# Kernel tuning notes

Hardware: AMD Instinct MI355X
Metric: run time of the kernel (lower is better)

Reference implementation:

```python
import jax, jax.numpy as jnp
import numpy as np

EMB_DIM = 1024
NUM_HEADS = 16
HEAD_DIM = EMB_DIM // NUM_HEADS
B, S = 2, 2048


def setup_inputs() -> dict:
    key = jax.random.key(0)
    k1, k2, k3, k4, k5, k6 = jax.random.split(key, 6)
    query = jax.random.normal(k1, (B, S, EMB_DIM), dtype=jnp.float32)
    key_t = jax.random.normal(k2, (B, S, EMB_DIM), dtype=jnp.float32)
    # causal mask: True above the diagonal = masked
    attention_mask = jnp.triu(jnp.ones((S, S), dtype=bool), k=1)
    scale = 1.0 / np.sqrt(EMB_DIM)
    Wq = jax.random.normal(k3, (EMB_DIM, EMB_DIM), dtype=jnp.float32) * scale
    Wk = jax.random.normal(k4, (EMB_DIM, EMB_DIM), dtype=jnp.float32) * scale
    Wv = jax.random.normal(k5, (EMB_DIM, EMB_DIM), dtype=jnp.float32) * scale
    Wo = jax.random.normal(k6, (EMB_DIM, EMB_DIM), dtype=jnp.float32) * scale
    return {"query": query, "key": key_t, "attention_mask": attention_mask,
            "Wq": Wq, "Wk": Wk, "Wv": Wv, "Wo": Wo}


def _split_heads(x):
    b, s, d = x.shape
    return x.reshape(b, s, NUM_HEADS, HEAD_DIM).transpose(0, 2, 1, 3)  # [B,H,S,hd]


def reference(query, key, attention_mask, Wq, Wk, Wv, Wo):
    # self-attention (encoder_decoder_attention=False): k,v come from query; `key` unused
    q = _split_heads(query @ Wq.T)
    k = _split_heads(query @ Wk.T)
    v = _split_heads(query @ Wv.T)
    scores = jnp.einsum('bhqd,bhkd->bhqk', q, k) / np.sqrt(HEAD_DIM)
    # causal=True: mask broadcast as [1,1,S,S]
    scores = jnp.where(attention_mask[None, None, :, :], -jnp.inf, scores)
    attn_weights = jax.nn.softmax(scores, axis=-1)  # [B,H,S,S]
    # dropout p=0.0 -> identity
    attn_out = jnp.einsum('bhqk,bhkd->bhqd', attn_weights, v)
    attn_out = attn_out.transpose(0, 2, 1, 3).reshape(query.shape[0], query.shape[1], EMB_DIM)
    attn_out = attn_out @ Wo.T
    return attn_out, attn_weights
```

## Files before the change

kernel.cpp:

```cpp
#include <hip/hip_runtime.h>
#include <stdint.h>

typedef __attribute__((ext_vector_type(8))) short bf16x8;
typedef __attribute__((ext_vector_type(4))) float f32x4;

#define MFMA16(a, b, c) __builtin_amdgcn_mfma_f32_16x16x32_bf16((a), (b), (c), 0, 0, 0)

static constexpr int NH = 16, HD = 64, SEQ = 2048, EMB = 1024;
static constexpr size_t O0 = (size_t)2 * SEQ * EMB;

__device__ __forceinline__ ushort f2bf(float f) {
  union { float f; uint32_t u; } v; v.f = f;
  uint32_t u = v.u;
  u = (u + 0x7fffu + ((u >> 16) & 1u)) >> 16;
  return (ushort)u;
}
__device__ __forceinline__ float bf2f(ushort h) {
  union { uint32_t u; float f; } v; v.u = ((uint32_t)h) << 16; return v.f;
}

__global__ void detect_kernel(const ushort* __restrict__ X, int* flag) {
  __shared__ int cnt;
  if (threadIdx.x == 0) cnt = 0;
  __syncthreads();
  int ok = 0;
  for (int i = 0; i < 16; ++i) {
    ushort w = X[threadIdx.x * 16 + i];
    int e = (w >> 7) & 0xFF;
    ok += (w == 0 || (e >= 100 && e <= 140)) ? 1 : 0;
  }
  atomicAdd(&cnt, ok);
  __syncthreads();
  if (threadIdx.x == 0) *flag = (cnt >= 3700) ? 0 : 1;
}

__global__ __launch_bounds__(256) void convert5(const void* __restrict__ x,
                                                const void* __restrict__ wq,
                                                const void* __restrict__ wk,
                                                const void* __restrict__ wv,
                                                const void* __restrict__ wo,
                                                ushort* __restrict__ Xb,
                                                ushort* __restrict__ Wb,
                                                const int* __restrict__ flagp) {
  const bool in32 = (*flagp) != 0;
  const size_t M = (size_t)1 << 20;
  const size_t gid = ((size_t)blockIdx.x * 256 + threadIdx.x) * 16;
  const void* src; ushort* dst; size_t off;
  if (gid < 4 * M)      { src = x;  off = gid;         dst = Xb + gid; }
  else if (gid < 5 * M) { src = wq; off = gid - 4 * M; dst = Wb + (gid - 4 * M); }
  else if (gid < 6 * M) { src = wk; off = gid - 5 * M; dst = Wb + (gid - 4 * M); }
  else if (gid < 7 * M) { src = wv; off = gid - 6 * M; dst = Wb + (gid - 4 * M); }
  else                  { src = wo; off = gid - 7 * M; dst = Wb + (gid - 4 * M); }
  if (in32) {
    const float4* p = reinterpret_cast<const float4*>((const float*)src + off);
    union { ushort h[16]; uint4 v[2]; } u;
#pragma unroll
    for (int j = 0; j < 4; ++j) {
      float4 fq = p[j];
      u.h[j * 4 + 0] = f2bf(fq.x); u.h[j * 4 + 1] = f2bf(fq.y);
      u.h[j * 4 + 2] = f2bf(fq.z); u.h[j * 4 + 3] = f2bf(fq.w);
    }
    *reinterpret_cast<uint4*>(dst)     = u.v[0];
    *reinterpret_cast<uint4*>(dst + 8) = u.v[1];
  } else {
    const uint4* p = reinterpret_cast<const uint4*>((const ushort*)src + off);
    *reinterpret_cast<uint4*>(dst)     = p[0];
    *reinterpret_cast<uint4*>(dst + 8) = p[1];
  }
}

__global__ __launch_bounds__(256, 3) void proj_qkv(const ushort* __restrict__ X,
                                                   const ushort* __restrict__ Wq,
                                                   const ushort* __restrict__ Wk,
                                                   const ushort* __restrict__ Wv,
                                                   ushort* __restrict__ Qws,
                                                   ushort* __restrict__ Kws,
                                                   ushort* __restrict__ Vtws) {
  __shared__ ushort As[128 * 72];
  __shared__ ushort Bs[128 * 72];
  const int t = threadIdx.x;
  const int wave = t >> 6, lane = t & 63, quad = lane >> 4, lr = lane & 15;
  const int wm = wave >> 1, wn = wave & 1;
  const int mBase = blockIdx.y * 128;
  const int nGlob = blockIdx.x * 128;
  const int which = nGlob >> 10;
  const int nBase = nGlob & 1023;
  const ushort* W = (which == 0) ? Wq : (which == 1) ? Wk : Wv;
  ushort* outp = (which == 0) ? Qws : (which == 1) ? Kws : Vtws;

  f32x4 acc[4][4];
  const f32x4 z4 = {0.f, 0.f, 0.f, 0.f};
#pragma unroll
  for (int mi = 0; mi < 4; ++mi)
#pragma unroll
    for (int ni = 0; ni < 4; ++ni) acc[mi][ni] = z4;

  for (int kb = 0; kb < 16; ++kb) {
    __syncthreads();
#pragma unroll
    for (int i = 0; i < 4; ++i) {
      int id = t + i * 256, r = id >> 3, c = id & 7;
      *reinterpret_cast<uint4*>(&As[r * 72 + c * 8]) =
          *reinterpret_cast<const uint4*>(X + (size_t)(mBase + r) * 1024 + kb * 64 + c * 8);
      *reinterpret_cast<uint4*>(&Bs[r * 72 + c * 8]) =
          *reinterpret_cast<const uint4*>(W + (size_t)(nBase + r) * 1024 + kb * 64 + c * 8);
    }
    __syncthreads();
#pragma unroll
    for (int ks = 0; ks < 2; ++ks) {
      bf16x8 af[4], bfr[4];
#pragma unroll
      for (int mi = 0; mi < 4; ++mi)
        af[mi] = *reinterpret_cast<const bf16x8*>(
            &As[(wm * 64 + mi * 16 + lr) * 72 + ks * 32 + quad * 8]);
#pragma unroll
      for (int ni = 0; ni < 4; ++ni)
        bfr[ni] = *reinterpret_cast<const bf16x8*>(
            &Bs[(wn * 64 + ni * 16 + lr) * 72 + ks * 32 + quad * 8]);
#pragma unroll
      for (int mi = 0; mi < 4; ++mi)
#pragma unroll
        for (int ni = 0; ni < 4; ++ni)
          acc[mi][ni] = MFMA16(af[mi], bfr[ni], acc[mi][ni]);
    }
  }

#pragma unroll
  for (int mi = 0; mi < 4; ++mi)
#pragma unroll
    for (int ni = 0; ni < 4; ++ni)
#pragma unroll
      for (int reg = 0; reg < 4; ++reg) {
        int m = mBase + wm * 64 + mi * 16 + quad * 4 + reg;
        int n = nBase + wn * 64 + ni * 16 + lr;
        int b = m >> 11, s = m & 2047, h = n >> 6, d = n & 63;
        size_t idx = (which == 2)
            ? ((size_t)(b * NH + h) * HD + d) * SEQ + s
            : ((size_t)(b * NH + h) * SEQ + s) * HD + d;
        outp[idx] = f2bf(acc[mi][ni][reg]);
      }
}

__global__ __launch_bounds__(256, 4) void proj_out(const ushort* __restrict__ A,
                                                   const ushort* __restrict__ W,
                                                   void* __restrict__ outp,
                                                   const int* __restrict__ flagp) {
  __shared__ ushort As[64 * 72];
  __shared__ ushort Bs[128 * 72];
  const bool f32io = (*flagp) != 0;
  const int t = threadIdx.x;
  const int wave = t >> 6, lane = t & 63, quad = lane >> 4, lr = lane & 15;
  const int wm = wave >> 1, wn = wave & 1;
  const int mBase = blockIdx.y * 64, nBase = blockIdx.x * 128;

  f32x4 acc[2][4];
  const f32x4 z4 = {0.f, 0.f, 0.f, 0.f};
#pragma unroll
  for (int mi = 0; mi < 2; ++mi)
#pragma unroll
    for (int ni = 0; ni < 4; ++ni) acc[mi][ni] = z4;

  for (int kb = 0; kb < 16; ++kb) {
    __syncthreads();
#pragma unroll
    for (int i = 0; i < 2; ++i) {
      int id = t + i * 256, r = id >> 3, c = id & 7;
      *reinterpret_cast<uint4*>(&As[r * 72 + c * 8]) =
          *reinterpret_cast<const uint4*>(A + (size_t)(mBase + r) * 1024 + kb * 64 + c * 8);
    }
#pragma unroll
    for (int i = 0; i < 4; ++i) {
      int id = t + i * 256, r = id >> 3, c = id & 7;
      *reinterpret_cast<uint4*>(&Bs[r * 72 + c * 8]) =
          *reinterpret_cast<const uint4*>(W + (size_t)(nBase + r) * 1024 + kb * 64 + c * 8);
    }
    __syncthreads();
#pragma unroll
    for (int ks = 0; ks < 2; ++ks) {
      bf16x8 af[2], bfr[4];
#pragma unroll
      for (int mi = 0; mi < 2; ++mi)
        af[mi] = *reinterpret_cast<const bf16x8*>(
            &As[(wm * 32 + mi * 16 + lr) * 72 + ks * 32 + quad * 8]);
#pragma unroll
      for (int ni = 0; ni < 4; ++ni)
        bfr[ni] = *reinterpret_cast<const bf16x8*>(
            &Bs[(wn * 64 + ni * 16 + lr) * 72 + ks * 32 + quad * 8]);
#pragma unroll
      for (int mi = 0; mi < 2; ++mi)
#pragma unroll
        for (int ni = 0; ni < 4; ++ni)
          acc[mi][ni] = MFMA16(af[mi], bfr[ni], acc[mi][ni]);
    }
  }

#pragma unroll
  for (int mi = 0; mi < 2; ++mi)
#pragma unroll
    for (int ni = 0; ni < 4; ++ni)
#pragma unroll
      for (int reg = 0; reg < 4; ++reg) {
        int m = mBase + wm * 32 + mi * 16 + quad * 4 + reg;
        int n = nBase + wn * 64 + ni * 16 + lr;
        size_t idx = (size_t)m * EMB + n;
        if (f32io) ((float*)outp)[idx] = acc[mi][ni][reg];
        else       ((ushort*)outp)[idx] = f2bf(acc[mi][ni][reg]);
      }
}

__global__ __launch_bounds__(256, 4) void attn_kernel(const ushort* __restrict__ Q,
                                                      const ushort* __restrict__ K,
                                                      const ushort* __restrict__ Vt,
                                                      void* __restrict__ dout,
                                                      ushort* __restrict__ Oout,
                                                      const int* __restrict__ flagp) {
  __shared__ ushort KVs[128 * 72];
  __shared__ ushort Ps[64 * 136];

  const int f = *flagp;
  const int t = threadIdx.x;
  const int wave = t >> 6, lane = t & 63, quad = lane >> 4, lr = lane & 15;
  const int bh = blockIdx.x, b = bh >> 4, h = bh & 15;
  const int sel = blockIdx.y, g = sel >> 3, r8 = sel & 7;
  const int qt = g * 8 + ((g & 1) ? r8 : 7 - r8);
  const int qBase = qt * 64;
  const int lastkt = qBase >> 7;

  const ushort* Qp = Q + (size_t)bh * SEQ * HD;
  const ushort* Kp = K + (size_t)bh * SEQ * HD;
  const ushort* Vp = Vt + (size_t)bh * HD * SEQ;
  ushort* P16 = (ushort*)dout + O0 + (size_t)bh * SEQ * SEQ;
  float*  P32 = (float*)dout + O0 + (size_t)bh * SEQ * SEQ;

#pragma unroll
  for (int i = 0; i < 2; ++i) {
    int id = t + i * 256, r = id >> 3, c = id & 7;
    *reinterpret_cast<uint4*>(&Ps[r * 72 + c * 8]) =
        *reinterpret_cast<const uint4*>(Qp + (size_t)(qBase + r) * HD + c * 8);
  }
  __syncthreads();
  bf16x8 qa[2];
#pragma unroll
  for (int ks = 0; ks < 2; ++ks)
    qa[ks] = *reinterpret_cast<const bf16x8*>(
        &Ps[(wave * 16 + lr) * 72 + ks * 32 + quad * 8]);

  if (f) {
    const float4 zf = make_float4(0.f, 0.f, 0.f, 0.f);
    for (int zt = lastkt + 1; zt < 16; ++zt)
#pragma unroll
      for (int i = 0; i < 8; ++i) {
        int id = t + i * 256, r = id >> 5, c = id & 31;
        *reinterpret_cast<float4*>(P32 + (size_t)(qBase + r) * SEQ + zt * 128 + c * 4) = zf;
      }
  } else {
    const uint4 zz = make_uint4(0, 0, 0, 0);
    for (int zt = lastkt + 1; zt < 16; ++zt)
#pragma unroll
      for (int i = 0; i < 4; ++i) {
        int id = t + i * 256, r = id >> 4, c = id & 15;
        *reinterpret_cast<uint4*>(P16 + (size_t)(qBase + r) * SEQ + zt * 128 + c * 8) = zz;
      }
  }

  float m_i[4], l_i[4], rl[4];
#pragma unroll
  for (int reg = 0; reg < 4; ++reg) { m_i[reg] = -1e9f; l_i[reg] = 0.f; }
  f32x4 oacc[4];
  const f32x4 z4 = {0.f, 0.f, 0.f, 0.f};
#pragma unroll
  for (int ni = 0; ni < 4; ++ni) oacc[ni] = z4;

  for (int pass = 0; pass < 2; ++pass) {
    if (pass == 1) {
#pragma unroll
      for (int reg = 0; reg < 4; ++reg) rl[reg] = 1.f / l_i[reg];
    }
    for (int kt = 0; kt <= lastkt; ++kt) {
      __syncthreads();
#pragma unroll
      for (int i = 0; i < 4; ++i) {
        int id = t + i * 256, r = id >> 3, c = id & 7;
        *reinterpret_cast<uint4*>(&KVs[r * 72 + c * 8]) =
            *reinterpret_cast<const uint4*>(Kp + (size_t)(kt * 128 + r) * HD + c * 8);
      }
      __syncthreads();

      f32x4 s[8];
#pragma unroll
      for (int ni = 0; ni < 8; ++ni) s[ni] = z4;
#pragma unroll
      for (int ni = 0; ni < 8; ++ni) {
        bf16x8 kb0 = *reinterpret_cast<const bf16x8*>(&KVs[(ni * 16 + lr) * 72 + quad * 8]);
        bf16x8 kb1 = *reinterpret_cast<const bf16x8*>(&KVs[(ni * 16 + lr) * 72 + 32 + quad * 8]);
        s[ni] = MFMA16(qa[0], kb0, s[ni]);
        s[ni] = MFMA16(qa[1], kb1, s[ni]);
      }
      const bool dm = (kt == lastkt);
#pragma unroll
      for (int ni = 0; ni < 8; ++ni)
#pragma unroll
        for (int reg = 0; reg < 4; ++reg) {
          float v = s[ni][reg] * 0.125f;
          if (dm) {
            int qg = qBase + wave * 16 + quad * 4 + reg;
            int kg = kt * 128 + ni * 16 + lr;
            if (kg > qg) v = -1e9f;
          }
          s[ni][reg] = v;
        }

      if (pass == 0) {
#pragma unroll
        for (int reg = 0; reg < 4; ++reg) {
          float tm = s[0][reg];
#pragma unroll
          for (int ni = 1; ni < 8; ++ni) tm = fmaxf(tm, s[ni][reg]);
#pragma unroll
          for (int off = 1; off < 16; off <<= 1) tm = fmaxf(tm, __shfl_xor(tm, off, 64));
          float mn = fmaxf(m_i[reg], tm);
          float ps = 0.f;
#pragma unroll
          for (int ni = 0; ni < 8; ++ni) ps += __expf(s[ni][reg] - mn);
#pragma unroll
          for (int off = 1; off < 16; off <<= 1) ps += __shfl_xor(ps, off, 64);
          l_i[reg] = l_i[reg] * __expf(m_i[reg] - mn) + ps;
          m_i[reg] = mn;
        }
      } else {
#pragma unroll
        for (int ni = 0; ni < 8; ++ni)
#pragma unroll
          for (int reg = 0; reg < 4; ++reg) {
            float p = __expf(s[ni][reg] - m_i[reg]) * rl[reg];
            Ps[(wave * 16 + quad * 4 + reg) * 136 + ni * 16 + lr] = f2bf(p);
          }
        __syncthreads();
        if (f) {
#pragma unroll
          for (int i = 0; i < 8; ++i) {
            int id = t + i * 256, r = id >> 5, c = id & 31;
            float4 o;
            o.x = bf2f(Ps[r * 136 + c * 4 + 0]);
            o.y = bf2f(Ps[r * 136 + c * 4 + 1]);
            o.z = bf2f(Ps[r * 136 + c * 4 + 2]);
            o.w = bf2f(Ps[r * 136 + c * 4 + 3]);
            *reinterpret_cast<float4*>(P32 + (size_t)(qBase + r) * SEQ + kt * 128 + c * 4) = o;
          }
        } else {
#pragma unroll
          for (int i = 0; i < 4; ++i) {
            int id = t + i * 256, r = id >> 4, c = id & 15;
            *reinterpret_cast<uint4*>(P16 + (size_t)(qBase + r) * SEQ + kt * 128 + c * 8) =
                *reinterpret_cast<const uint4*>(&Ps[r * 136 + c * 8]);
          }
        }
#pragma unroll
        for (int i = 0; i < 4; ++i) {
          int id = t + i * 256, r = id >> 4, c = id & 15;
          *reinterpret_cast<uint4*>(&KVs[r * 136 + c * 8]) =
              *reinterpret_cast<const uint4*>(Vp + (size_t)r * SEQ + kt * 128 + c * 8);
        }
        __syncthreads();
#pragma unroll
        for (int ks2 = 0; ks2 < 4; ++ks2) {
          bf16x8 pa = *reinterpret_cast<const bf16x8*>(
              &Ps[(wave * 16 + lr) * 136 + ks2 * 32 + quad * 8]);
#pragma unroll
          for (int ni = 0; ni < 4; ++ni) {
            bf16x8 vb = *reinterpret_cast<const bf16x8*>(
                &KVs[(ni * 16 + lr) * 136 + ks2 * 32 + quad * 8]);
            oacc[ni] = MFMA16(pa, vb, oacc[ni]);
          }
        }
      }
    }
  }

#pragma unroll
  for (int ni = 0; ni < 4; ++ni)
#pragma unroll
    for (int reg = 0; reg < 4; ++reg) {
      int r = wave * 16 + quad * 4 + reg;
      int d = ni * 16 + lr;
      Oout[((size_t)(b * SEQ + qBase + r)) * EMB + h * HD + d] = f2bf(oacc[ni][reg]);
    }
}

extern "C" void kernel_launch(void* const* d_in, const int* in_sizes, int n_in,
                              void* d_out, int out_size, void* d_ws, size_t ws_size,
                              hipStream_t stream) {
  const size_t SZ = (size_t)2 * NH * SEQ * HD;
  int* flag    = (int*)d_ws;
  ushort* Qws  = (ushort*)((char*)d_ws + 256);
  ushort* Kws  = Qws + SZ;
  ushort* Vtws = Kws + SZ;
  ushort* Ows  = Vtws + SZ;
  ushort* Xb   = Ows;
  ushort* Wb   = Ows + SZ;

  detect_kernel<<<1, 256, 0, stream>>>((const ushort*)d_in[0], flag);
  convert5<<<2048, 256, 0, stream>>>(d_in[0], d_in[3], d_in[4], d_in[5], d_in[6],
                                     Xb, Wb, flag);
  proj_qkv<<<dim3(24, 32), 256, 0, stream>>>(Xb, Wb, Wb + (1u << 20), Wb + (2u << 20),
                                             Qws, Kws, Vtws);
  attn_kernel<<<dim3(32, 32), 256, 0, stream>>>(Qws, Kws, Vtws, d_out, Ows, flag);
  proj_out<<<dim3(8, 64), 256, 0, stream>>>(Ows, Wb + (3u << 20), d_out, flag);
}
```

Before: 839.9 us.

## Software-pipeline K/V tile loads with register prefetch and double-buffered LDS

Splits the two-pass softmax loop into two explicit loops. In the stats pass, the next K tile is prefetched into registers while the current tile is computed, and tiles alternate between two LDS buffers (KVs and an XOR-swizzled view of Ps), so each iteration needs only one barrier. In the output pass, the next K tile and the current V tile are loaded into registers ahead of the MFMA and softmax work to hide global latency. This adds register pressure under launch_bounds(256,4) and makes the LDS buffer reuse more intricate.

Result: slower. 911.4 us (+8.5%).

```diff
diff --git a/kernel.cpp b/kernel.cpp
--- a/kernel.cpp
+++ b/kernel.cpp
@@ -214,8 +214,8 @@
                                                       void* __restrict__ dout,
                                                       ushort* __restrict__ Oout,
                                                       const int* __restrict__ flagp) {
-  __shared__ ushort KVs[128 * 72];
-  __shared__ ushort Ps[64 * 136];
+  __shared__ __align__(16) ushort KVs[128 * 72];
+  __shared__ __align__(16) ushort Ps[64 * 136];
 
   const int f = *flagp;
   const int t = threadIdx.x;
@@ -271,30 +271,47 @@
 #pragma unroll
   for (int ni = 0; ni < 4; ++ni) oacc[ni] = z4;
 
-  for (int pass = 0; pass < 2; ++pass) {
-    if (pass == 1) {
-#pragma unroll
-      for (int reg = 0; reg < 4; ++reg) rl[reg] = 1.f / l_i[reg];
+  {
+#pragma unroll
+    for (int i = 0; i < 4; ++i) {
+      int id = t + i * 256, r = id >> 3, c = id & 7;
+      *reinterpret_cast<uint4*>(&KVs[r * 72 + c * 8]) =
+          *reinterpret_cast<const uint4*>(Kp + (size_t)r * HD + c * 8);
     }
     for (int kt = 0; kt <= lastkt; ++kt) {
       __syncthreads();
-#pragma unroll
-      for (int i = 0; i < 4; ++i) {
-        int id = t + i * 256, r = id >> 3, c = id & 7;
-        *reinterpret_cast<uint4*>(&KVs[r * 72 + c * 8]) =
-            *reinterpret_cast<const uint4*>(Kp + (size_t)(kt * 128 + r) * HD + c * 8);
-      }
-      __syncthreads();
-
+      uint4 kst[4];
+      const bool pre = (kt < lastkt);
+      if (pre) {
+#pragma unroll
+        for (int i = 0; i < 4; ++i) {
+          int id = t + i * 256, r = id >> 3, c = id & 7;
+          kst[i] = *reinterpret_cast<const uint4*>(
+              Kp + (size_t)((kt + 1) * 128 + r) * HD + c * 8);
+        }
+      }
       f32x4 s[8];
 #pragma unroll
       for (int ni = 0; ni < 8; ++ni) s[ni] = z4;
-#pragma unroll
-      for (int ni = 0; ni < 8; ++ni) {
-        bf16x8 kb0 = *reinterpret_cast<const bf16x8*>(&KVs[(ni * 16 + lr) * 72 + quad * 8]);
-        bf16x8 kb1 = *reinterpret_cast<const bf16x8*>(&KVs[(ni * 16 + lr) * 72 + 32 + quad * 8]);
-        s[ni] = MFMA16(qa[0], kb0, s[ni]);
-        s[ni] = MFMA16(qa[1], kb1, s[ni]);
+      if (!(kt & 1)) {
+#pragma unroll
+        for (int ni = 0; ni < 8; ++ni) {
+          bf16x8 kb0 = *reinterpret_cast<const bf16x8*>(&KVs[(ni * 16 + lr) * 72 + quad * 8]);
+          bf16x8 kb1 = *reinterpret_cast<const bf16x8*>(&KVs[(ni * 16 + lr) * 72 + 32 + quad * 8]);
+          s[ni] = MFMA16(qa[0], kb0, s[ni]);
+          s[ni] = MFMA16(qa[1], kb1, s[ni]);
+        }
+      } else {
+        const char* base = reinterpret_cast<const char*>(Ps);
+        const int xm = (lr & 7) << 4;
+#pragma unroll
+        for (int ni = 0; ni < 8; ++ni) {
+          int row = ni * 16 + lr;
+          bf16x8 kb0 = *reinterpret_cast<const bf16x8*>(base + ((row * 128 + quad * 16) ^ xm));
+          bf16x8 kb1 = *reinterpret_cast<const bf16x8*>(base + ((row * 128 + 64 + quad * 16) ^ xm));
+          s[ni] = MFMA16(qa[0], kb0, s[ni]);
+          s[ni] = MFMA16(qa[1], kb1, s[ni]);
+        }
       }
       const bool dm = (kt == lastkt);
 #pragma unroll
@@ -309,69 +326,137 @@
           }
           s[ni][reg] = v;
         }
-
-      if (pass == 0) {
-#pragma unroll
-        for (int reg = 0; reg < 4; ++reg) {
-          float tm = s[0][reg];
-#pragma unroll
-          for (int ni = 1; ni < 8; ++ni) tm = fmaxf(tm, s[ni][reg]);
-#pragma unroll
-          for (int off = 1; off < 16; off <<= 1) tm = fmaxf(tm, __shfl_xor(tm, off, 64));
-          float mn = fmaxf(m_i[reg], tm);
-          float ps = 0.f;
-#pragma unroll
-          for (int ni = 0; ni < 8; ++ni) ps += __expf(s[ni][reg] - mn);
-#pragma unroll
-          for (int off = 1; off < 16; off <<= 1) ps += __shfl_xor(ps, off, 64);
-          l_i[reg] = l_i[reg] * __expf(m_i[reg] - mn) + ps;
-          m_i[reg] = mn;
-        }
-      } else {
-#pragma unroll
-        for (int ni = 0; ni < 8; ++ni)
-#pragma unroll
-          for (int reg = 0; reg < 4; ++reg) {
-            float p = __expf(s[ni][reg] - m_i[reg]) * rl[reg];
-            Ps[(wave * 16 + quad * 4 + reg) * 136 + ni * 16 + lr] = f2bf(p);
-          }
-        __syncthreads();
-        if (f) {
-#pragma unroll
-          for (int i = 0; i < 8; ++i) {
-            int id = t + i * 256, r = id >> 5, c = id & 31;
-            float4 o;
-            o.x = bf2f(Ps[r * 136 + c * 4 + 0]);
-            o.y = bf2f(Ps[r * 136 + c * 4 + 1]);
-            o.z = bf2f(Ps[r * 136 + c * 4 + 2]);
-            o.w = bf2f(Ps[r * 136 + c * 4 + 3]);
-            *reinterpret_cast<float4*>(P32 + (size_t)(qBase + r) * SEQ + kt * 128 + c * 4) = o;
+#pragma unroll
+      for (int reg = 0; reg < 4; ++reg) {
+        float tm = s[0][reg];
+#pragma unroll
+        for (int ni = 1; ni < 8; ++ni) tm = fmaxf(tm, s[ni][reg]);
+#pragma unroll
+        for (int off = 1; off < 16; off <<= 1) tm = fmaxf(tm, __shfl_xor(tm, off, 64));
+        float mn = fmaxf(m_i[reg], tm);
+        float ps = 0.f;
+#pragma unroll
+        for (int ni = 0; ni < 8; ++ni) ps += __expf(s[ni][reg] - mn);
+#pragma unroll
+        for (int off = 1; off < 16; off <<= 1) ps += __shfl_xor(ps, off, 64);
+        l_i[reg] = l_i[reg] * __expf(m_i[reg] - mn) + ps;
+        m_i[reg] = mn;
+      }
+      if (pre) {
+        if (!((kt + 1) & 1)) {
+#pragma unroll
+          for (int i = 0; i < 4; ++i) {
+            int id = t + i * 256, r = id >> 3, c = id & 7;
+            *reinterpret_cast<uint4*>(&KVs[r * 72 + c * 8]) = kst[i];
           }
         } else {
+          char* base = reinterpret_cast<char*>(Ps);
 #pragma unroll
           for (int i = 0; i < 4; ++i) {
-            int id = t + i * 256, r = id >> 4, c = id & 15;
-            *reinterpret_cast<uint4*>(P16 + (size_t)(qBase + r) * SEQ + kt * 128 + c * 8) =
-                *reinterpret_cast<const uint4*>(&Ps[r * 136 + c * 8]);
+            int id = t + i * 256, r = id >> 3, c = id & 7;
+            *reinterpret_cast<uint4*>(base + ((r * 128 + c * 16) ^ ((r & 7) << 4))) = kst[i];
           }
         }
+      }
+    }
+  }
+
+#pragma unroll
+  for (int reg = 0; reg < 4; ++reg) rl[reg] = 1.f / l_i[reg];
+
+  {
+    uint4 kst[4], vst[4];
+#pragma unroll
+    for (int i = 0; i < 4; ++i) {
+      int id = t + i * 256, r = id >> 3, c = id & 7;
+      kst[i] = *reinterpret_cast<const uint4*>(Kp + (size_t)r * HD + c * 8);
+    }
+    for (int kt = 0; kt <= lastkt; ++kt) {
+      __syncthreads();
+#pragma unroll
+      for (int i = 0; i < 4; ++i) {
+        int id = t + i * 256, r = id >> 3, c = id & 7;
+        *reinterpret_cast<uint4*>(&KVs[r * 72 + c * 8]) = kst[i];
+      }
+      __syncthreads();
+#pragma unroll
+      for (int i = 0; i < 4; ++i) {
+        int id = t + i * 256, r = id >> 4, c = id & 15;
+        vst[i] = *reinterpret_cast<const uint4*>(Vp + (size_t)r * SEQ + kt * 128 + c * 8);
+      }
+      if (kt < lastkt) {
+#pragma unroll
+        for (int i = 0; i < 4; ++i) {
+          int id = t + i * 256, r = id >> 3, c = id & 7;
+          kst[i] = *reinterpret_cast<const uint4*>(
+              Kp + (size_t)((kt + 1) * 128 + r) * HD + c * 8);
+        }
+      }
+      f32x4 s[8];
+#pragma unroll
+      for (int ni = 0; ni < 8; ++ni) s[ni] = z4;
+#pragma unroll
+      for (int ni = 0; ni < 8; ++ni) {
+        bf16x8 kb0 = *reinterpret_cast<const bf16x8*>(&KVs[(ni * 16 + lr) * 72 + quad * 8]);
+        bf16x8 kb1 = *reinterpret_cast<const bf16x8*>(&KVs[(ni * 16 + lr) * 72 + 32 + quad * 8]);
+        s[ni] = MFMA16(qa[0], kb0, s[ni]);
+        s[ni] = MFMA16(qa[1], kb1, s[ni]);
+      }
+      const bool dm = (kt == lastkt);
+#pragma unroll
+      for (int ni = 0; ni < 8; ++ni)
+#pragma unroll
+        for (int reg = 0; reg < 4; ++reg) {
+          float v = s[ni][reg] * 0.125f;
+          if (dm) {
+            int qg = qBase + wave * 16 + quad * 4 + reg;
+            int kg = kt * 128 + ni * 16 + lr;
+            if (kg > qg) v = -1e9f;
+          }
+          s[ni][reg] = v;
+        }
+#pragma unroll
+      for (int ni = 0; ni < 8; ++ni)
+#pragma unroll
+        for (int reg = 0; reg < 4; ++reg) {
+          float p = __expf(s[ni][reg] - m_i[reg]) * rl[reg];
+          Ps[(wave * 16 + quad * 4 + reg) * 136 + ni * 16 + lr] = f2bf(p);
+        }
+      __syncthreads();
+#pragma unroll
+      for (int i = 0; i < 4; ++i) {
+        int id = t + i * 256, r = id >> 4, c = id & 15;
+        *reinterpret_cast<uint4*>(&KVs[r * 136 + c * 8]) = vst[i];
+      }
+      if (f) {
+#pragma unroll
+        for (int i = 0; i < 8; ++i) {
+          int id = t + i * 256, r = id >> 5, c = id & 31;
+          float4 o;
+          o.x = bf2f(Ps[r * 136 + c * 4 + 0]);
+          o.y = bf2f(Ps[r * 136 + c * 4 + 1]);
+          o.z = bf2f(Ps[r * 136 + c * 4 + 2]);
+          o.w = bf2f(Ps[r * 136 + c * 4 + 3]);
+          *reinterpret_cast<float4*>(P32 + (size_t)(qBase + r) * SEQ + kt * 128 + c * 4) = o;
+        }
+      } else {
 #pragma unroll
         for (int i = 0; i < 4; ++i) {
           int id = t + i * 256, r = id >> 4, c = id & 15;
-          *reinterpret_cast<uint4*>(&KVs[r * 136 + c * 8]) =
-              *reinterpret_cast<const uint4*>(Vp + (size_t)r * SEQ + kt * 128 + c * 8);
-        }
-        __syncthreads();
-#pragma unroll
-        for (int ks2 = 0; ks2 < 4; ++ks2) {
-          bf16x8 pa = *reinterpret_cast<const bf16x8*>(
-              &Ps[(wave * 16 + lr) * 136 + ks2 * 32 + quad * 8]);
-#pragma unroll
-          for (int ni = 0; ni < 4; ++ni) {
-            bf16x8 vb = *reinterpret_cast<const bf16x8*>(
-                &KVs[(ni * 16 + lr) * 136 + ks2 * 32 + quad * 8]);
-            oacc[ni] = MFMA16(pa, vb, oacc[ni]);
-          }
+          *reinterpret_cast<uint4*>(P16 + (size_t)(qBase + r) * SEQ + kt * 128 + c * 8) =
+              *reinterpret_cast<const uint4*>(&Ps[r * 136 + c * 8]);
+        }
+      }
+      __syncthreads();
+#pragma unroll
+      for (int ks2 = 0; ks2 < 4; ++ks2) {
+        bf16x8 pa = *reinterpret_cast<const bf16x8*>(
+            &Ps[(wave * 16 + lr) * 136 + ks2 * 32 + quad * 8]);
+#pragma unroll
+        for (int ni = 0; ni < 4; ++ni) {
+          bf16x8 vb = *reinterpret_cast<const bf16x8*>(
+              &KVs[(ni * 16 + lr) * 136 + ks2 * 32 + quad * 8]);
+          oacc[ni] = MFMA16(pa, vb, oacc[ni]);
         }
       }
     }
```

## Use direct global-to-LDS loads with XOR swizzle and double-buffer attention K pass

Applied to the files above, without the earlier changes.

Replaces register-staged global-to-shared copies in the QKV and output projection GEMMs with global_load_lds 16-byte direct loads into an XOR-swizzled unpadded LDS layout. In attention, the first (max/sum) pass now prefetches the next K tile asynchronously into a second buffer that reuses the P buffer, and the second pass loads K via direct-to-LDS and issues the V load before the P stores. The aim is to cut VGPR traffic and load latency and to overlap K fetch with QK compute. It relies on the swizzle matching between the per-lane write pattern and the reads, and on correct ordering of the async LDS writes around barriers.

After: 746.3 us. 1.13x faster.

```diff
diff --git a/kernel.cpp b/kernel.cpp
--- a/kernel.cpp
+++ b/kernel.cpp
@@ -17,6 +17,12 @@
 }
 __device__ __forceinline__ float bf2f(ushort h) {
   union { uint32_t u; float f; } v; v.u = ((uint32_t)h) << 16; return v.f;
+}
+
+__device__ __forceinline__ void glds16(const void* gp, void* lp) {
+  __builtin_amdgcn_global_load_lds(
+      (const __attribute__((address_space(1))) unsigned int*)gp,
+      (__attribute__((address_space(3))) unsigned int*)lp, 16, 0, 0);
 }
 
 __global__ void detect_kernel(const ushort* __restrict__ X, int* flag) {
@@ -76,8 +82,8 @@
                                                    ushort* __restrict__ Qws,
                                                    ushort* __restrict__ Kws,
                                                    ushort* __restrict__ Vtws) {
-  __shared__ ushort As[128 * 72];
-  __shared__ ushort Bs[128 * 72];
+  __shared__ __align__(16) char As[128 * 128];
+  __shared__ __align__(16) char Bs[128 * 128];
   const int t = threadIdx.x;
   const int wave = t >> 6, lane = t & 63, quad = lane >> 4, lr = lane & 15;
   const int wm = wave >> 1, wn = wave & 1;
@@ -95,28 +101,37 @@
 #pragma unroll
     for (int ni = 0; ni < 4; ++ni) acc[mi][ni] = z4;
 
+  const int row0 = lane >> 3;
+  const int inrow = (((lane & 7) ^ (lane >> 3)) & 7) << 4;
+  const int xm = (lr & 7) << 4;
+
   for (int kb = 0; kb < 16; ++kb) {
     __syncthreads();
 #pragma unroll
     for (int i = 0; i < 4; ++i) {
-      int id = t + i * 256, r = id >> 3, c = id & 7;
-      *reinterpret_cast<uint4*>(&As[r * 72 + c * 8]) =
-          *reinterpret_cast<const uint4*>(X + (size_t)(mBase + r) * 1024 + kb * 64 + c * 8);
-      *reinterpret_cast<uint4*>(&Bs[r * 72 + c * 8]) =
-          *reinterpret_cast<const uint4*>(W + (size_t)(nBase + r) * 1024 + kb * 64 + c * 8);
+      int ch = wave * 4 + i;
+      int row = ch * 8 + row0;
+      glds16((const char*)X + ((size_t)(mBase + row) * 2048 + kb * 128 + inrow),
+             As + ch * 1024);
+      glds16((const char*)W + ((size_t)(nBase + row) * 2048 + kb * 128 + inrow),
+             Bs + ch * 1024);
     }
     __syncthreads();
 #pragma unroll
     for (int ks = 0; ks < 2; ++ks) {
       bf16x8 af[4], bfr[4];
 #pragma unroll
-      for (int mi = 0; mi < 4; ++mi)
+      for (int mi = 0; mi < 4; ++mi) {
+        int rw = wm * 64 + mi * 16 + lr;
         af[mi] = *reinterpret_cast<const bf16x8*>(
-            &As[(wm * 64 + mi * 16 + lr) * 72 + ks * 32 + quad * 8]);
-#pragma unroll
-      for (int ni = 0; ni < 4; ++ni)
+            As + rw * 128 + ((ks * 64 + quad * 16) ^ xm));
+      }
+#pragma unroll
+      for (int ni = 0; ni < 4; ++ni) {
+        int rw = wn * 64 + ni * 16 + lr;
         bfr[ni] = *reinterpret_cast<const bf16x8*>(
-            &Bs[(wn * 64 + ni * 16 + lr) * 72 + ks * 32 + quad * 8]);
+            Bs + rw * 128 + ((ks * 64 + quad * 16) ^ xm));
+      }
 #pragma unroll
       for (int mi = 0; mi < 4; ++mi)
 #pragma unroll
@@ -145,8 +160,8 @@
                                                    const ushort* __restrict__ W,
                                                    void* __restrict__ outp,
                                                    const int* __restrict__ flagp) {
-  __shared__ ushort As[64 * 72];
-  __shared__ ushort Bs[128 * 72];
+  __shared__ __align__(16) char As[64 * 128];
+  __shared__ __align__(16) char Bs[128 * 128];
   const bool f32io = (*flagp) != 0;
   const int t = threadIdx.x;
   const int wave = t >> 6, lane = t & 63, quad = lane >> 4, lr = lane & 15;
@@ -160,32 +175,42 @@
 #pragma unroll
     for (int ni = 0; ni < 4; ++ni) acc[mi][ni] = z4;
 
+  const int row0 = lane >> 3;
+  const int inrow = (((lane & 7) ^ (lane >> 3)) & 7) << 4;
+  const int xm = (lr & 7) << 4;
+
   for (int kb = 0; kb < 16; ++kb) {
     __syncthreads();
 #pragma unroll
     for (int i = 0; i < 2; ++i) {
-      int id = t + i * 256, r = id >> 3, c = id & 7;
-      *reinterpret_cast<uint4*>(&As[r * 72 + c * 8]) =
-          *reinterpret_cast<const uint4*>(A + (size_t)(mBase + r) * 1024 + kb * 64 + c * 8);
+      int ch = wave * 2 + i;
+      int row = ch * 8 + row0;
+      glds16((const char*)A + ((size_t)(mBase + row) * 2048 + kb * 128 + inrow),
+             As + ch * 1024);
     }
 #pragma unroll
     for (int i = 0; i < 4; ++i) {
-      int id = t + i * 256, r = id >> 3, c = id & 7;
-      *reinterpret_cast<uint4*>(&Bs[r * 72 + c * 8]) =
-          *reinterpret_cast<const uint4*>(W + (size_t)(nBase + r) * 1024 + kb * 64 + c * 8);
+      int ch = wave * 4 + i;
+      int row = ch * 8 + row0;
+      glds16((const char*)W + ((size_t)(nBase + row) * 2048 + kb * 128 + inrow),
+             Bs + ch * 1024);
     }
     __syncthreads();
 #pragma unroll
     for (int ks = 0; ks < 2; ++ks) {
       bf16x8 af[2], bfr[4];
 #pragma unroll
-      for (int mi = 0; mi < 2; ++mi)
+      for (int mi = 0; mi < 2; ++mi) {
+        int rw = wm * 32 + mi * 16 + lr;
         af[mi] = *reinterpret_cast<const bf16x8*>(
-            &As[(wm * 32 + mi * 16 + lr) * 72 + ks * 32 + quad * 8]);
-#pragma unroll
-      for (int ni = 0; ni < 4; ++ni)
+            As + rw * 128 + ((ks * 64 + quad * 16) ^ xm));
+      }
+#pragma unroll
+      for (int ni = 0; ni < 4; ++ni) {
+        int rw = wn * 64 + ni * 16 + lr;
         bfr[ni] = *reinterpret_cast<const bf16x8*>(
-            &Bs[(wn * 64 + ni * 16 + lr) * 72 + ks * 32 + quad * 8]);
+            Bs + rw * 128 + ((ks * 64 + quad * 16) ^ xm));
+      }
 #pragma unroll
       for (int mi = 0; mi < 2; ++mi)
 #pragma unroll
@@ -214,8 +239,8 @@
                                                       void* __restrict__ dout,
                                                       ushort* __restrict__ Oout,
                                                       const int* __restrict__ flagp) {
-  __shared__ ushort KVs[128 * 72];
-  __shared__ ushort Ps[64 * 136];
+  __shared__ __align__(16) ushort KVs[128 * 72];
+  __shared__ __align__(16) ushort Ps[64 * 136];
 
   const int f = *flagp;
   const int t = threadIdx.x;
@@ -232,6 +257,10 @@
   ushort* P16 = (ushort*)dout + O0 + (size_t)bh * SEQ * SEQ;
   float*  P32 = (float*)dout + O0 + (size_t)bh * SEQ * SEQ;
 
+  const int row0 = lane >> 3;
+  const int inrow = (((lane & 7) ^ (lane >> 3)) & 7) << 4;
+  const int xm = (lr & 7) << 4;
+
 #pragma unroll
   for (int i = 0; i < 2; ++i) {
     int id = t + i * 256, r = id >> 3, c = id & 7;
@@ -271,28 +300,34 @@
 #pragma unroll
   for (int ni = 0; ni < 4; ++ni) oacc[ni] = z4;
 
-  for (int pass = 0; pass < 2; ++pass) {
-    if (pass == 1) {
-#pragma unroll
-      for (int reg = 0; reg < 4; ++reg) rl[reg] = 1.f / l_i[reg];
+  {
+#pragma unroll
+    for (int i = 0; i < 4; ++i) {
+      int ch = wave * 4 + i;
+      int row = ch * 8 + row0;
+      glds16((const char*)Kp + (size_t)row * 128 + inrow, (char*)KVs + ch * 1024);
     }
     for (int kt = 0; kt <= lastkt; ++kt) {
       __syncthreads();
-#pragma unroll
-      for (int i = 0; i < 4; ++i) {
-        int id = t + i * 256, r = id >> 3, c = id & 7;
-        *reinterpret_cast<uint4*>(&KVs[r * 72 + c * 8]) =
-            *reinterpret_cast<const uint4*>(Kp + (size_t)(kt * 128 + r) * HD + c * 8);
-      }
-      __syncthreads();
-
+      if (kt < lastkt) {
+        char* nb = ((kt + 1) & 1) ? (char*)Ps : (char*)KVs;
+        const char* tb = (const char*)Kp + (size_t)(kt + 1) * 16384;
+#pragma unroll
+        for (int i = 0; i < 4; ++i) {
+          int ch = wave * 4 + i;
+          int row = ch * 8 + row0;
+          glds16(tb + (size_t)row * 128 + inrow, nb + ch * 1024);
+        }
+      }
+      const char* kb = (kt & 1) ? (const char*)Ps : (const char*)KVs;
       f32x4 s[8];
 #pragma unroll
       for (int ni = 0; ni < 8; ++ni) s[ni] = z4;
 #pragma unroll
       for (int ni = 0; ni < 8; ++ni) {
-        bf16x8 kb0 = *reinterpret_cast<const bf16x8*>(&KVs[(ni * 16 + lr) * 72 + quad * 8]);
-        bf16x8 kb1 = *reinterpret_cast<const bf16x8*>(&KVs[(ni * 16 + lr) * 72 + 32 + quad * 8]);
+        int rw = ni * 16 + lr;
+        bf16x8 kb0 = *reinterpret_cast<const bf16x8*>(kb + rw * 128 + ((quad * 16) ^ xm));
+        bf16x8 kb1 = *reinterpret_cast<const bf16x8*>(kb + rw * 128 + ((64 + quad * 16) ^ xm));
         s[ni] = MFMA16(qa[0], kb0, s[ni]);
         s[ni] = MFMA16(qa[1], kb1, s[ni]);
       }
@@ -309,70 +344,106 @@
           }
           s[ni][reg] = v;
         }
-
-      if (pass == 0) {
-#pragma unroll
-        for (int reg = 0; reg < 4; ++reg) {
-          float tm = s[0][reg];
-#pragma unroll
-          for (int ni = 1; ni < 8; ++ni) tm = fmaxf(tm, s[ni][reg]);
-#pragma unroll
-          for (int off = 1; off < 16; off <<= 1) tm = fmaxf(tm, __shfl_xor(tm, off, 64));
-          float mn = fmaxf(m_i[reg], tm);
-          float ps = 0.f;
-#pragma unroll
-          for (int ni = 0; ni < 8; ++ni) ps += __expf(s[ni][reg] - mn);
-#pragma unroll
-          for (int off = 1; off < 16; off <<= 1) ps += __shfl_xor(ps, off, 64);
-          l_i[reg] = l_i[reg] * __expf(m_i[reg] - mn) + ps;
-          m_i[reg] = mn;
+#pragma unroll
+      for (int reg = 0; reg < 4; ++reg) {
+        float tm = s[0][reg];
+#pragma unroll
+        for (int ni = 1; ni < 8; ++ni) tm = fmaxf(tm, s[ni][reg]);
+#pragma unroll
+        for (int off = 1; off < 16; off <<= 1) tm = fmaxf(tm, __shfl_xor(tm, off, 64));
+        float mn = fmaxf(m_i[reg], tm);
+        float ps = 0.f;
+#pragma unroll
+        for (int ni = 0; ni < 8; ++ni) ps += __expf(s[ni][reg] - mn);
+#pragma unroll
+        for (int off = 1; off < 16; off <<= 1) ps += __shfl_xor(ps, off, 64);
+        l_i[reg] = l_i[reg] * __expf(m_i[reg] - mn) + ps;
+        m_i[reg] = mn;
+      }
+    }
+  }
+
+#pragma unroll
+  for (int reg = 0; reg < 4; ++reg) rl[reg] = 1.f / l_i[reg];
+
+  for (int kt = 0; kt <= lastkt; ++kt) {
+    __syncthreads();
+#pragma unroll
+    for (int i = 0; i < 4; ++i) {
+      int ch = wave * 4 + i;
+      int row = ch * 8 + row0;
+      glds16((const char*)Kp + (size_t)kt * 16384 + (size_t)row * 128 + inrow,
+             (char*)KVs + ch * 1024);
+    }
+    __syncthreads();
+    f32x4 s[8];
+#pragma unroll
+    for (int ni = 0; ni < 8; ++ni) s[ni] = z4;
+#pragma unroll
+    for (int ni = 0; ni < 8; ++ni) {
+      int rw = ni * 16 + lr;
+      const char* kb = (const char*)KVs;
+      bf16x8 kb0 = *reinterpret_cast<const bf16x8*>(kb + rw * 128 + ((quad * 16) ^ xm));
+      bf16x8 kb1 = *reinterpret_cast<const bf16x8*>(kb + rw * 128 + ((64 + quad * 16) ^ xm));
+      s[ni] = MFMA16(qa[0], kb0, s[ni]);
+      s[ni] = MFMA16(qa[1], kb1, s[ni]);
+    }
+    const bool dm = (kt == lastkt);
+#pragma unroll
+    for (int ni = 0; ni < 8; ++ni)
+#pragma unroll
+      for (int reg = 0; reg < 4; ++reg) {
+        float v = s[ni][reg] * 0.125f;
+        if (dm) {
+          int qg = qBase + wave * 16 + quad * 4 + reg;
+          int kg = kt * 128 + ni * 16 + lr;
+          if (kg > qg) v = -1e9f;
         }
-      } else {
-#pragma unroll
-        for (int ni = 0; ni < 8; ++ni)
-#pragma unroll
-          for (int reg = 0; reg < 4; ++reg) {
-            float p = __expf(s[ni][reg] - m_i[reg]) * rl[reg];
-            Ps[(wave * 16 + quad * 4 + reg) * 136 + ni * 16 + lr] = f2bf(p);
-          }
-        __syncthreads();
-        if (f) {
-#pragma unroll
-          for (int i = 0; i < 8; ++i) {
-            int id = t + i * 256, r = id >> 5, c = id & 31;
-            float4 o;
-            o.x = bf2f(Ps[r * 136 + c * 4 + 0]);
-            o.y = bf2f(Ps[r * 136 + c * 4 + 1]);
-            o.z = bf2f(Ps[r * 136 + c * 4 + 2]);
-            o.w = bf2f(Ps[r * 136 + c * 4 + 3]);
-            *reinterpret_cast<float4*>(P32 + (size_t)(qBase + r) * SEQ + kt * 128 + c * 4) = o;
-          }
-        } else {
-#pragma unroll
-          for (int i = 0; i < 4; ++i) {
-            int id = t + i * 256, r = id >> 4, c = id & 15;
-            *reinterpret_cast<uint4*>(P16 + (size_t)(qBase + r) * SEQ + kt * 128 + c * 8) =
-                *reinterpret_cast<const uint4*>(&Ps[r * 136 + c * 8]);
-          }
-        }
-#pragma unroll
-        for (int i = 0; i < 4; ++i) {
-          int id = t + i * 256, r = id >> 4, c = id & 15;
-          *reinterpret_cast<uint4*>(&KVs[r * 136 + c * 8]) =
-              *reinterpret_cast<const uint4*>(Vp + (size_t)r * SEQ + kt * 128 + c * 8);
-        }
-        __syncthreads();
-#pragma unroll
-        for (int ks2 = 0; ks2 < 4; ++ks2) {
-          bf16x8 pa = *reinterpret_cast<const bf16x8*>(
-              &Ps[(wave * 16 + lr) * 136 + ks2 * 32 + quad * 8]);
-#pragma unroll
-          for (int ni = 0; ni < 4; ++ni) {
-            bf16x8 vb = *reinterpret_cast<const bf16x8*>(
-                &KVs[(ni * 16 + lr) * 136 + ks2 * 32 + quad * 8]);
-            oacc[ni] = MFMA16(pa, vb, oacc[ni]);
-          }
-        }
+        s[ni][reg] = v;
+      }
+#pragma unroll
+    for (int ni = 0; ni < 8; ++ni)
+#pragma unroll
+      for (int reg = 0; reg < 4; ++reg) {
+        float p = __expf(s[ni][reg] - m_i[reg]) * rl[reg];
+        Ps[(wave * 16 + quad * 4 + reg) * 136 + ni * 16 + lr] = f2bf(p);
+      }
+    __syncthreads();
+#pragma unroll
+    for (int i = 0; i < 4; ++i) {
+      int id = t + i * 256, r = id >> 4, c = id & 15;
+      *reinterpret_cast<uint4*>(&KVs[r * 136 + c * 8]) =
+          *reinterpret_cast<const uint4*>(Vp + (size_t)r * SEQ + kt * 128 + c * 8);
+    }
+    if (f) {
+#pragma unroll
+      for (int i = 0; i < 8; ++i) {
+        int id = t + i * 256, r = id >> 5, c = id & 31;
+        float4 o;
+        o.x = bf2f(Ps[r * 136 + c * 4 + 0]);
+        o.y = bf2f(Ps[r * 136 + c * 4 + 1]);
+        o.z = bf2f(Ps[r * 136 + c * 4 + 2]);
+        o.w = bf2f(Ps[r * 136 + c * 4 + 3]);
+        *reinterpret_cast<float4*>(P32 + (size_t)(qBase + r) * SEQ + kt * 128 + c * 4) = o;
+      }
+    } else {
+#pragma unroll
+      for (int i = 0; i < 4; ++i) {
+        int id = t + i * 256, r = id >> 4, c = id & 15;
+        *reinterpret_cast<uint4*>(P16 + (size_t)(qBase + r) * SEQ + kt * 128 + c * 8) =
+            *reinterpret_cast<const uint4*>(&Ps[r * 136 + c * 8]);
+      }
+    }
+    __syncthreads();
+#pragma unroll
+    for (int ks2 = 0; ks2 < 4; ++ks2) {
+      bf16x8 pa = *reinterpret_cast<const bf16x8*>(
+          &Ps[(wave * 16 + lr) * 136 + ks2 * 32 + quad * 8]);
+#pragma unroll
+      for (int ni = 0; ni < 4; ++ni) {
+        bf16x8 vb = *reinterpret_cast<const bf16x8*>(
+            &KVs[(ni * 16 + lr) * 136 + ks2 * 32 + quad * 8]);
+        oacc[ni] = MFMA16(pa, vb, oacc[ni]);
       }
     }
   }
```
